# Kernel tuning notes

Hardware: AMD Instinct MI355X
Metric: run time of the kernel (lower is better)

## Reference

```python
import jax, jax.numpy as jnp
import numpy as np

D_MODEL = 1024
N_HEADS = 16
D_HEAD = 64


def setup_inputs() -> dict:
    key = jax.random.key(0)
    kx, kq, kk, kv, ko = jax.random.split(key, 5)
    B, T = 2, 2048
    inner = N_HEADS * D_HEAD
    s = 1.0 / np.sqrt(D_MODEL)
    return {
        "x": jax.random.normal(kx, (B, T, D_MODEL), dtype=jnp.float32),
        "Wq": jax.random.normal(kq, (D_MODEL, inner), dtype=jnp.float32) * s,
        "Wk": jax.random.normal(kk, (D_MODEL, inner), dtype=jnp.float32) * s,
        "Wv": jax.random.normal(kv, (D_MODEL, inner), dtype=jnp.float32) * s,
        "Wo": jax.random.normal(ko, (inner, D_MODEL), dtype=jnp.float32) * (1.0 / np.sqrt(inner)),
    }


def reference(x, Wq, Wk, Wv, Wo):
    B, T, D = x.shape
    H, d = N_HEADS, D_HEAD
    q = (x @ Wq).reshape(B, T, H, d)
    k = (x @ Wk).reshape(B, T, H, d)
    v = (x @ Wv).reshape(B, T, H, d)
    # scale=False -> no 1/sqrt(d) scaling
    scores = jnp.einsum('bthd,bshd->bhts', q, k)
    # strictly-lower-triangular mask (tril with diagonal=-1): s < t kept
    mask = jnp.tril(jnp.ones((T, T), dtype=bool), k=-1)
    scores = jnp.where(mask, scores, 0.0)
    out = jnp.einsum('bhts,bshd->bthd', scores, v).reshape(B, T, H * d)
    return out @ Wo
```

## Files before the change

### kernel.cpp

```cpp
#include <hip/hip_runtime.h>
#include <hip/hip_bf16.h>

#define TSEQ   2048
#define DM     1024
#define NHEAD  16
#define DH     64
#define BATCH  2
#define MR     (BATCH * TSEQ)
#define CH     64
#define NC     (TSEQ / CH)
#define QKVLD  (3 * DM)
#define LP     72

typedef __attribute__((ext_vector_type(8))) short bf16x8;
typedef __attribute__((ext_vector_type(4))) float f32x4;

__device__ __forceinline__ short f2bf(float x) {
  __hip_bfloat16 h = __float2bfloat16(x);
  return *reinterpret_cast<short*>(&h);
}

__device__ __forceinline__ void stage16(const void* g, void* l) {
  __builtin_amdgcn_global_load_lds(
      (const __attribute__((address_space(1))) void*)g,
      (__attribute__((address_space(3))) void*)l, 16, 0, 0);
}

__global__ __launch_bounds__(256) void gemm_qkv(const short* __restrict__ A,
                                                const short* __restrict__ Bt,
                                                short* __restrict__ qb,
                                                short* __restrict__ kb,
                                                short* __restrict__ kT,
                                                short* __restrict__ vT) {
  const int K = DM;
  __shared__ short As[128][32];
  __shared__ short Bs[128][32];
  const int tid = threadIdx.x;
  const int lane = tid & 63, wid = tid >> 6;
  const int wave_m = wid >> 1, wave_n = wid & 1;
  const int row0 = blockIdx.y * 128, col0 = blockIdx.x * 128;

  const int sr = tid >> 2, sk = (tid & 3) * 8;
  const short* Ag0 = A + (size_t)(row0 + sr) * K + sk;
  const short* Bg0 = Bt + (size_t)(col0 + sr) * K + sk;
  short* AsL = &As[0][0] + tid * 8;
  short* BsL = &Bs[0][0] + tid * 8;

  f32x4 acc[4][4];
#pragma unroll
  for (int i = 0; i < 4; ++i)
#pragma unroll
    for (int j = 0; j < 4; ++j) acc[i][j] = (f32x4){0.f, 0.f, 0.f, 0.f};

  const int fm = wave_m * 64 + (lane & 15);
  const int fn = wave_n * 64 + (lane & 15);
  const int fk = (lane >> 4) * 8;

  for (int k0 = 0; k0 < K; k0 += 32) {
    stage16(Ag0 + k0, AsL);
    stage16(Ag0 + (size_t)64 * K + k0, AsL + 2048);
    stage16(Bg0 + k0, BsL);
    stage16(Bg0 + (size_t)64 * K + k0, BsL + 2048);
    __syncthreads();
    bf16x8 af[4], bf[4];
#pragma unroll
    for (int t = 0; t < 4; ++t) {
      af[t] = *(const bf16x8*)&As[fm + t * 16][fk];
      bf[t] = *(const bf16x8*)&Bs[fn + t * 16][fk];
    }
#pragma unroll
    for (int im = 0; im < 4; ++im)
#pragma unroll
      for (int jn = 0; jn < 4; ++jn)
        acc[im][jn] = __builtin_amdgcn_mfma_f32_16x16x32_bf16(af[im], bf[jn], acc[im][jn], 0, 0, 0);
    __syncthreads();
  }

  const int crow = (lane >> 4) * 4, ccol = lane & 15;
  const int region = col0 >> 10;

  if (region <= 1) {
    short* Cb = (region == 0) ? qb : kb;
#pragma unroll
    for (int im = 0; im < 4; ++im)
#pragma unroll
      for (int jn = 0; jn < 4; ++jn) {
        const int gr = row0 + wave_m * 64 + im * 16 + crow;
        const int gc = (col0 & 1023) + wave_n * 64 + jn * 16 + ccol;
        short* Cp = Cb + (size_t)gr * DM + gc;
#pragma unroll
        for (int r = 0; r < 4; ++r) Cp[(size_t)r * DM] = f2bf(acc[im][jn][r]);
      }
  }
  if (region >= 1) {
    short* Tt = (region == 1) ? kT : vT;
    const int gr0 = row0 + wave_m * 64;
    const int b = gr0 >> 11;
    const int c = (gr0 & 2047) >> 6;
#pragma unroll
    for (int im = 0; im < 4; ++im)
#pragma unroll
      for (int jn = 0; jn < 4; ++jn) {
        const int gcol = (col0 & 1023) + wave_n * 64 + jn * 16 + ccol;
        const int h = gcol >> 6, i = gcol & 63;
        const int s0 = im * 16 + crow;
        size_t idx = ((((size_t)(b * NHEAD + h) * NC + c) * DH + i) * DH + s0);
        union { short h4[4]; uint2 u; } pk;
#pragma unroll
        for (int r = 0; r < 4; ++r) pk.h4[r] = f2bf(acc[im][jn][r]);
        *(uint2*)(Tt + idx) = pk.u;
      }
  }
}

__global__ __launch_bounds__(256) void gemm_out(const short* __restrict__ A,
                                                const short* __restrict__ Bt,
                                                float* __restrict__ C) {
  const int K = DM, N = DM;
  __shared__ short As[128][32];
  __shared__ short Bs[128][32];
  const int tid = threadIdx.x;
  const int lane = tid & 63, wid = tid >> 6;
  const int wave_m = wid >> 1, wave_n = wid & 1;
  const int row0 = blockIdx.y * 128, col0 = blockIdx.x * 128;

  const int sr = tid >> 2, sk = (tid & 3) * 8;
  const short* Ag0 = A + (size_t)(row0 + sr) * K + sk;
  const short* Bg0 = Bt + (size_t)(col0 + sr) * K + sk;
  short* AsL = &As[0][0] + tid * 8;
  short* BsL = &Bs[0][0] + tid * 8;

  f32x4 acc[4][4];
#pragma unroll
  for (int i = 0; i < 4; ++i)
#pragma unroll
    for (int j = 0; j < 4; ++j) acc[i][j] = (f32x4){0.f, 0.f, 0.f, 0.f};

  const int fm = wave_m * 64 + (lane & 15);
  const int fn = wave_n * 64 + (lane & 15);
  const int fk = (lane >> 4) * 8;

  for (int k0 = 0; k0 < K; k0 += 32) {
    stage16(Ag0 + k0, AsL);
    stage16(Ag0 + (size_t)64 * K + k0, AsL + 2048);
    stage16(Bg0 + k0, BsL);
    stage16(Bg0 + (size_t)64 * K + k0, BsL + 2048);
    __syncthreads();
    bf16x8 af[4], bf[4];
#pragma unroll
    for (int t = 0; t < 4; ++t) {
      af[t] = *(const bf16x8*)&As[fm + t * 16][fk];
      bf[t] = *(const bf16x8*)&Bs[fn + t * 16][fk];
    }
#pragma unroll
    for (int im = 0; im < 4; ++im)
#pragma unroll
      for (int jn = 0; jn < 4; ++jn)
        acc[im][jn] = __builtin_amdgcn_mfma_f32_16x16x32_bf16(af[im], bf[jn], acc[im][jn], 0, 0, 0);
    __syncthreads();
  }

  const int crow = (lane >> 4) * 4, ccol = lane & 15;
#pragma unroll
  for (int im = 0; im < 4; ++im)
#pragma unroll
    for (int jn = 0; jn < 4; ++jn) {
      float* Cp = C + (size_t)(row0 + wave_m * 64 + im * 16 + crow) * N
                    + col0 + wave_n * 64 + jn * 16 + ccol;
#pragma unroll
      for (int r = 0; r < 4; ++r) Cp[(size_t)r * N] = acc[im][jn][r];
    }
}

__global__ __launch_bounds__(256) void prep(const float* __restrict__ x,
                                            const float* __restrict__ W0,
                                            const float* __restrict__ W1,
                                            const float* __restrict__ W2,
                                            const float* __restrict__ W3,
                                            __hip_bfloat16* __restrict__ xb,
                                            __hip_bfloat16* __restrict__ Wt) {
  const int tid = threadIdx.x;
  if (blockIdx.z == 4) {
    const int bid = blockIdx.y * 16 + blockIdx.x;
    const float* src = x + (size_t)bid * 16384;
    __hip_bfloat16* dst = xb + (size_t)bid * 16384;
#pragma unroll
    for (int it = 0; it < 16; ++it) {
      int i = it * 1024 + tid * 4;
      float4 v = *(const float4*)(src + i);
      union { __hip_bfloat16 h[4]; uint2 u; } pk;
      pk.h[0] = __float2bfloat16(v.x); pk.h[1] = __float2bfloat16(v.y);
      pk.h[2] = __float2bfloat16(v.z); pk.h[3] = __float2bfloat16(v.w);
      *(uint2*)(dst + i) = pk.u;
    }
    return;
  }
  const float* W = blockIdx.z == 0 ? W0 : blockIdx.z == 1 ? W1 : blockIdx.z == 2 ? W2 : W3;
  __hip_bfloat16* out = Wt + (size_t)blockIdx.z * DM * DM;
  __shared__ float tile[64][65];
  const int kt = blockIdx.y * 64, nt = blockIdx.x * 64;
  const int lr = tid >> 6, lc = tid & 63;
#pragma unroll
  for (int i = 0; i < 16; ++i) {
    int k = i * 4 + lr;
    tile[k][lc] = W[(size_t)(kt + k) * DM + nt + lc];
  }
  __syncthreads();
  const int nl = tid >> 4, k4 = (tid & 15) * 4;
#pragma unroll
  for (int i = 0; i < 4; ++i) {
    int n = i * 16 + nl;
    union { __hip_bfloat16 h[4]; uint2 u; } pk;
#pragma unroll
    for (int xx = 0; xx < 4; ++xx) pk.h[xx] = __float2bfloat16(tile[k4 + xx][n]);
    *(uint2*)(out + (size_t)(nt + n) * DM + kt + k4) = pk.u;
  }
}

__global__ __launch_bounds__(256) void chunk_kv(const short* __restrict__ kT,
                                                const short* __restrict__ vT,
                                                float* __restrict__ Mc) {
  const int c = blockIdx.x, h = blockIdx.y, b = blockIdx.z;
  const size_t tile = ((size_t)(b * NHEAD + h) * NC + c) * (DH * DH);
  const int tid = threadIdx.x, lane = tid & 63, w = tid >> 6;
  const int m = lane & 15, q = lane >> 4;
  const short* vt = vT + tile;
  const short* kt = kT + tile;
  bf16x8 a0 = *(const bf16x8*)(vt + (16 * w + m) * DH + q * 8);
  bf16x8 a1 = *(const bf16x8*)(vt + (16 * w + m) * DH + q * 8 + 32);
  f32x4 acc[4];
#pragma unroll
  for (int ct = 0; ct < 4; ++ct) acc[ct] = (f32x4){0.f, 0.f, 0.f, 0.f};
#pragma unroll
  for (int ct = 0; ct < 4; ++ct) {
    bf16x8 b0 = *(const bf16x8*)(kt + (ct * 16 + m) * DH + q * 8);
    bf16x8 b1 = *(const bf16x8*)(kt + (ct * 16 + m) * DH + q * 8 + 32);
    acc[ct] = __builtin_amdgcn_mfma_f32_16x16x32_bf16(a0, b0, acc[ct], 0, 0, 0);
    acc[ct] = __builtin_amdgcn_mfma_f32_16x16x32_bf16(a1, b1, acc[ct], 0, 0, 0);
  }
  float* out = Mc + tile;
#pragma unroll
  for (int ct = 0; ct < 4; ++ct)
#pragma unroll
    for (int rr = 0; rr < 4; ++rr)
      out[(size_t)(16 * w + q * 4 + rr) * DH + ct * 16 + m] = acc[ct][rr];
}

__global__ __launch_bounds__(256) void scan_states(const float* __restrict__ Mc,
                                                   __hip_bfloat16* __restrict__ Spre) {
  const int bh = blockIdx.y;
  const size_t off = (size_t)bh * NC * (DH * DH) + blockIdx.x * 256 + threadIdx.x;
  const float* src = Mc + off;
  __hip_bfloat16* dst = Spre + off;
  float run = 0.f;
  for (int c = 0; c < NC; ++c) {
    dst[(size_t)c * (DH * DH)] = __float2bfloat16(run);
    run += src[(size_t)c * (DH * DH)];
  }
}

__global__ __launch_bounds__(256) void intra_attn(const short* __restrict__ qb,
                                                  const short* __restrict__ kb,
                                                  const short* __restrict__ vT,
                                                  const short* __restrict__ Spre,
                                                  short* __restrict__ O_) {
  const int c = blockIdx.x, h = blockIdx.y, b = blockIdx.z;
  __shared__ short Qs[CH][LP];
  __shared__ short Ks[CH][LP];
  const int tid = threadIdx.x, lane = tid & 63, w = tid >> 6;
  const int m = lane & 15, q = lane >> 4;
  const int r = tid >> 2, q16 = (tid & 3) * 16;
  const size_t tile = ((size_t)(b * NHEAD + h) * NC + c) * (DH * DH);
  const size_t grow = ((size_t)(b * TSEQ + c * CH + r)) * DM + h * DH;
  *(bf16x8*)&Qs[r][q16]     = *(const bf16x8*)(qb + grow + q16);
  *(bf16x8*)&Qs[r][q16 + 8] = *(const bf16x8*)(qb + grow + q16 + 8);
  *(bf16x8*)&Ks[r][q16]     = *(const bf16x8*)(kb + grow + q16);
  *(bf16x8*)&Ks[r][q16 + 8] = *(const bf16x8*)(kb + grow + q16 + 8);
  const short* vt = vT + tile;
  const short* st = Spre + tile;
  bf16x8 av0 = *(const bf16x8*)(vt + (16 * w + m) * DH + q * 8);
  bf16x8 av1 = *(const bf16x8*)(vt + (16 * w + m) * DH + q * 8 + 32);
  bf16x8 as0 = *(const bf16x8*)(st + (16 * w + m) * DH + q * 8);
  bf16x8 as1 = *(const bf16x8*)(st + (16 * w + m) * DH + q * 8 + 32);
  __syncthreads();

  bf16x8 aq0 = *(const bf16x8*)&Qs[16 * w + m][q * 8];
  bf16x8 aq1 = *(const bf16x8*)&Qs[16 * w + m][q * 8 + 32];

  f32x4 acc[4], pacc[4];
#pragma unroll
  for (int ct = 0; ct < 4; ++ct) {
    acc[ct] = (f32x4){0.f, 0.f, 0.f, 0.f};
    pacc[ct] = (f32x4){0.f, 0.f, 0.f, 0.f};
  }
#pragma unroll
  for (int ct = 0; ct < 4; ++ct) {
    bf16x8 bq0 = *(const bf16x8*)&Qs[ct * 16 + m][q * 8];
    bf16x8 bq1 = *(const bf16x8*)&Qs[ct * 16 + m][q * 8 + 32];
    acc[ct] = __builtin_amdgcn_mfma_f32_16x16x32_bf16(as0, bq0, acc[ct], 0, 0, 0);
    acc[ct] = __builtin_amdgcn_mfma_f32_16x16x32_bf16(as1, bq1, acc[ct], 0, 0, 0);
    bf16x8 bk0 = *(const bf16x8*)&Ks[ct * 16 + m][q * 8];
    bf16x8 bk1 = *(const bf16x8*)&Ks[ct * 16 + m][q * 8 + 32];
    pacc[ct] = __builtin_amdgcn_mfma_f32_16x16x32_bf16(aq0, bk0, pacc[ct], 0, 0, 0);
    pacc[ct] = __builtin_amdgcn_mfma_f32_16x16x32_bf16(aq1, bk1, pacc[ct], 0, 0, 0);
  }
  __syncthreads();
#pragma unroll
  for (int ct = 0; ct < 4; ++ct) {
    const int s = ct * 16 + m;
#pragma unroll
    for (int rr = 0; rr < 4; ++rr) {
      const int t = 16 * w + q * 4 + rr;
      Ks[t][s] = f2bf((s < t) ? pacc[ct][rr] : 0.f);
    }
  }
  __syncthreads();
#pragma unroll
  for (int ct = 0; ct < 4; ++ct) {
    bf16x8 bp0 = *(const bf16x8*)&Ks[ct * 16 + m][q * 8];
    bf16x8 bp1 = *(const bf16x8*)&Ks[ct * 16 + m][q * 8 + 32];
    acc[ct] = __builtin_amdgcn_mfma_f32_16x16x32_bf16(av0, bp0, acc[ct], 0, 0, 0);
    acc[ct] = __builtin_amdgcn_mfma_f32_16x16x32_bf16(av1, bp1, acc[ct], 0, 0, 0);
  }
#pragma unroll
  for (int ct = 0; ct < 4; ++ct) {
    const int t = ct * 16 + m, j0 = 16 * w + q * 4;
    union { short h4[4]; uint2 u; } pk;
#pragma unroll
    for (int rr = 0; rr < 4; ++rr) pk.h4[rr] = f2bf(acc[ct][rr]);
    *(uint2*)(O_ + ((size_t)(b * TSEQ + c * CH + t)) * DM + h * DH + j0) = pk.u;
  }
}

extern "C" void kernel_launch(void* const* d_in, const int* in_sizes, int n_in,
                              void* d_out, int out_size, void* d_ws, size_t ws_size,
                              hipStream_t stream) {
  const float* x  = (const float*)d_in[0];
  const float* Wq = (const float*)d_in[1];
  const float* Wk = (const float*)d_in[2];
  const float* Wv = (const float*)d_in[3];
  const float* Wo = (const float*)d_in[4];
  float* out = (float*)d_out;

  char* ws = (char*)d_ws;
  short* xb    = (short*)ws;  ws += (size_t)MR * DM * 2;
  short* WtAll = (short*)ws;  ws += (size_t)4 * DM * DM * 2;
  short* qb    = (short*)ws;  ws += (size_t)MR * DM * 2;
  short* kb    = (short*)ws;  ws += (size_t)MR * DM * 2;
  short* kT    = (short*)ws;  ws += (size_t)MR * DM * 2;
  short* vT    = (short*)ws;  ws += (size_t)MR * DM * 2;
  float* Mc    = (float*)ws;  ws += (size_t)MR * DM * 4;
  short* Spre  = (short*)ws;  ws += (size_t)MR * DM * 2;
  short* aob   = (short*)ws;  ws += (size_t)MR * DM * 2;

  prep<<<dim3(16, 16, 5), 256, 0, stream>>>(x, Wq, Wk, Wv, Wo,
                                            (__hip_bfloat16*)xb, (__hip_bfloat16*)WtAll);

  gemm_qkv<<<dim3(QKVLD / 128, MR / 128), 256, 0, stream>>>(xb, WtAll, qb, kb, kT, vT);

  chunk_kv<<<dim3(NC, NHEAD, BATCH), 256, 0, stream>>>(kT, vT, Mc);
  scan_states<<<dim3(DH * DH / 256, BATCH * NHEAD), 256, 0, stream>>>(
      Mc, (__hip_bfloat16*)Spre);
  intra_attn<<<dim3(NC, NHEAD, BATCH), 256, 0, stream>>>(qb, kb, vT, Spre, aob);

  gemm_out<<<dim3(DM / 128, MR / 128), 256, 0, stream>>>(
      aob, WtAll + (size_t)3 * DM * DM, out);
}
```

Baseline: 170.8 us.

## Fuse chunk state computation with prefix scan, deepen QKV GEMM K-step, shrink out-GEMM tile

The separate chunk_kv and scan_states kernels become one state_scan kernel. It computes each chunk's K^T V contribution with MFMA and keeps the running prefix sum in registers, so the fp32 Mc buffer no longer has to be written and read back. The QKV GEMM now stages 64 K-columns per barrier pair, halving the number of synchronisations. The output GEMM uses 128x64 tiles so twice as many blocks launch for better occupancy. The trade-off is that state_scan runs only 128 blocks that walk the chunks sequentially, which limits parallelism.

```diff
diff --git a/kernel.cpp b/kernel.cpp
--- a/kernel.cpp
+++ b/kernel.cpp
@@ -33,8 +33,8 @@
                                                 short* __restrict__ kT,
                                                 short* __restrict__ vT) {
   const int K = DM;
-  __shared__ short As[128][32];
-  __shared__ short Bs[128][32];
+  __shared__ short As[2][128][32];
+  __shared__ short Bs[2][128][32];
   const int tid = threadIdx.x;
   const int lane = tid & 63, wid = tid >> 6;
   const int wave_m = wid >> 1, wave_n = wid & 1;
@@ -43,8 +43,8 @@
   const int sr = tid >> 2, sk = (tid & 3) * 8;
   const short* Ag0 = A + (size_t)(row0 + sr) * K + sk;
   const short* Bg0 = Bt + (size_t)(col0 + sr) * K + sk;
-  short* AsL = &As[0][0] + tid * 8;
-  short* BsL = &Bs[0][0] + tid * 8;
+  short* AsL = &As[0][0][0] + tid * 8;
+  short* BsL = &Bs[0][0][0] + tid * 8;
 
   f32x4 acc[4][4];
 #pragma unroll
@@ -56,23 +56,30 @@
   const int fn = wave_n * 64 + (lane & 15);
   const int fk = (lane >> 4) * 8;
 
-  for (int k0 = 0; k0 < K; k0 += 32) {
+  for (int k0 = 0; k0 < K; k0 += 64) {
     stage16(Ag0 + k0, AsL);
     stage16(Ag0 + (size_t)64 * K + k0, AsL + 2048);
+    stage16(Ag0 + k0 + 32, AsL + 4096);
+    stage16(Ag0 + (size_t)64 * K + k0 + 32, AsL + 6144);
     stage16(Bg0 + k0, BsL);
     stage16(Bg0 + (size_t)64 * K + k0, BsL + 2048);
+    stage16(Bg0 + k0 + 32, BsL + 4096);
+    stage16(Bg0 + (size_t)64 * K + k0 + 32, BsL + 6144);
     __syncthreads();
-    bf16x8 af[4], bf[4];
-#pragma unroll
-    for (int t = 0; t < 4; ++t) {
-      af[t] = *(const bf16x8*)&As[fm + t * 16][fk];
-      bf[t] = *(const bf16x8*)&Bs[fn + t * 16][fk];
+#pragma unroll
+    for (int p = 0; p < 2; ++p) {
+      bf16x8 af[4], bf[4];
+#pragma unroll
+      for (int t = 0; t < 4; ++t) {
+        af[t] = *(const bf16x8*)&As[p][fm + t * 16][fk];
+        bf[t] = *(const bf16x8*)&Bs[p][fn + t * 16][fk];
+      }
+#pragma unroll
+      for (int im = 0; im < 4; ++im)
+#pragma unroll
+        for (int jn = 0; jn < 4; ++jn)
+          acc[im][jn] = __builtin_amdgcn_mfma_f32_16x16x32_bf16(af[im], bf[jn], acc[im][jn], 0, 0, 0);
     }
-#pragma unroll
-    for (int im = 0; im < 4; ++im)
-#pragma unroll
-      for (int jn = 0; jn < 4; ++jn)
-        acc[im][jn] = __builtin_amdgcn_mfma_f32_16x16x32_bf16(af[im], bf[jn], acc[im][jn], 0, 0, 0);
     __syncthreads();
   }
 
@@ -118,11 +125,9 @@
                                                 float* __restrict__ C) {
   const int K = DM, N = DM;
   __shared__ short As[128][32];
-  __shared__ short Bs[128][32];
-  const int tid = threadIdx.x;
-  const int lane = tid & 63, wid = tid >> 6;
-  const int wave_m = wid >> 1, wave_n = wid & 1;
-  const int row0 = blockIdx.y * 128, col0 = blockIdx.x * 128;
+  __shared__ short Bs[64][32];
+  const int tid = threadIdx.x, lane = tid & 63, wid = tid >> 6;
+  const int row0 = blockIdx.y * 128, col0 = blockIdx.x * 64;
 
   const int sr = tid >> 2, sk = (tid & 3) * 8;
   const short* Ag0 = A + (size_t)(row0 + sr) * K + sk;
@@ -130,30 +135,28 @@
   short* AsL = &As[0][0] + tid * 8;
   short* BsL = &Bs[0][0] + tid * 8;
 
-  f32x4 acc[4][4];
-#pragma unroll
-  for (int i = 0; i < 4; ++i)
+  f32x4 acc[2][4];
+#pragma unroll
+  for (int i = 0; i < 2; ++i)
 #pragma unroll
     for (int j = 0; j < 4; ++j) acc[i][j] = (f32x4){0.f, 0.f, 0.f, 0.f};
 
-  const int fm = wave_m * 64 + (lane & 15);
-  const int fn = wave_n * 64 + (lane & 15);
+  const int fm = wid * 32 + (lane & 15);
+  const int fn = lane & 15;
   const int fk = (lane >> 4) * 8;
 
   for (int k0 = 0; k0 < K; k0 += 32) {
     stage16(Ag0 + k0, AsL);
     stage16(Ag0 + (size_t)64 * K + k0, AsL + 2048);
     stage16(Bg0 + k0, BsL);
-    stage16(Bg0 + (size_t)64 * K + k0, BsL + 2048);
     __syncthreads();
-    bf16x8 af[4], bf[4];
-#pragma unroll
-    for (int t = 0; t < 4; ++t) {
-      af[t] = *(const bf16x8*)&As[fm + t * 16][fk];
-      bf[t] = *(const bf16x8*)&Bs[fn + t * 16][fk];
-    }
-#pragma unroll
-    for (int im = 0; im < 4; ++im)
+    bf16x8 af[2], bf[4];
+#pragma unroll
+    for (int t = 0; t < 2; ++t) af[t] = *(const bf16x8*)&As[fm + t * 16][fk];
+#pragma unroll
+    for (int t = 0; t < 4; ++t) bf[t] = *(const bf16x8*)&Bs[t * 16 + fn][fk];
+#pragma unroll
+    for (int im = 0; im < 2; ++im)
 #pragma unroll
       for (int jn = 0; jn < 4; ++jn)
         acc[im][jn] = __builtin_amdgcn_mfma_f32_16x16x32_bf16(af[im], bf[jn], acc[im][jn], 0, 0, 0);
@@ -162,11 +165,11 @@
 
   const int crow = (lane >> 4) * 4, ccol = lane & 15;
 #pragma unroll
-  for (int im = 0; im < 4; ++im)
+  for (int im = 0; im < 2; ++im)
 #pragma unroll
     for (int jn = 0; jn < 4; ++jn) {
-      float* Cp = C + (size_t)(row0 + wave_m * 64 + im * 16 + crow) * N
-                    + col0 + wave_n * 64 + jn * 16 + ccol;
+      float* Cp = C + (size_t)(row0 + wid * 32 + im * 16 + crow) * N
+                    + col0 + jn * 16 + ccol;
 #pragma unroll
       for (int r = 0; r < 4; ++r) Cp[(size_t)r * N] = acc[im][jn][r];
     }
@@ -217,45 +220,29 @@
   }
 }
 
-__global__ __launch_bounds__(256) void chunk_kv(const short* __restrict__ kT,
-                                                const short* __restrict__ vT,
-                                                float* __restrict__ Mc) {
-  const int c = blockIdx.x, h = blockIdx.y, b = blockIdx.z;
-  const size_t tile = ((size_t)(b * NHEAD + h) * NC + c) * (DH * DH);
+__global__ __launch_bounds__(256) void state_scan(const short* __restrict__ kT,
+                                                  const short* __restrict__ vT,
+                                                  short* __restrict__ Spre) {
+  const int js = blockIdx.x, h = blockIdx.y, b = blockIdx.z;
   const int tid = threadIdx.x, lane = tid & 63, w = tid >> 6;
   const int m = lane & 15, q = lane >> 4;
-  const short* vt = vT + tile;
-  const short* kt = kT + tile;
-  bf16x8 a0 = *(const bf16x8*)(vt + (16 * w + m) * DH + q * 8);
-  bf16x8 a1 = *(const bf16x8*)(vt + (16 * w + m) * DH + q * 8 + 32);
-  f32x4 acc[4];
-#pragma unroll
-  for (int ct = 0; ct < 4; ++ct) acc[ct] = (f32x4){0.f, 0.f, 0.f, 0.f};
-#pragma unroll
-  for (int ct = 0; ct < 4; ++ct) {
-    bf16x8 b0 = *(const bf16x8*)(kt + (ct * 16 + m) * DH + q * 8);
-    bf16x8 b1 = *(const bf16x8*)(kt + (ct * 16 + m) * DH + q * 8 + 32);
-    acc[ct] = __builtin_amdgcn_mfma_f32_16x16x32_bf16(a0, b0, acc[ct], 0, 0, 0);
-    acc[ct] = __builtin_amdgcn_mfma_f32_16x16x32_bf16(a1, b1, acc[ct], 0, 0, 0);
-  }
-  float* out = Mc + tile;
-#pragma unroll
-  for (int ct = 0; ct < 4; ++ct)
+  const size_t hbase = ((size_t)(b * NHEAD + h) * NC) * (DH * DH);
+  const int jrow = 16 * js + m;
+  const int irow = 16 * w + m;
+  f32x4 run = (f32x4){0.f, 0.f, 0.f, 0.f};
+  for (int c = 0; c < NC; ++c) {
+    const size_t tile = hbase + (size_t)c * (DH * DH);
 #pragma unroll
     for (int rr = 0; rr < 4; ++rr)
-      out[(size_t)(16 * w + q * 4 + rr) * DH + ct * 16 + m] = acc[ct][rr];
-}
-
-__global__ __launch_bounds__(256) void scan_states(const float* __restrict__ Mc,
-                                                   __hip_bfloat16* __restrict__ Spre) {
-  const int bh = blockIdx.y;
-  const size_t off = (size_t)bh * NC * (DH * DH) + blockIdx.x * 256 + threadIdx.x;
-  const float* src = Mc + off;
-  __hip_bfloat16* dst = Spre + off;
-  float run = 0.f;
-  for (int c = 0; c < NC; ++c) {
-    dst[(size_t)c * (DH * DH)] = __float2bfloat16(run);
-    run += src[(size_t)c * (DH * DH)];
+      Spre[tile + (size_t)(16 * js + q * 4 + rr) * DH + 16 * w + m] = f2bf(run[rr]);
+    bf16x8 a0 = *(const bf16x8*)(vT + tile + (size_t)jrow * DH + q * 8);
+    bf16x8 a1 = *(const bf16x8*)(vT + tile + (size_t)jrow * DH + q * 8 + 32);
+    bf16x8 b0 = *(const bf16x8*)(kT + tile + (size_t)irow * DH + q * 8);
+    bf16x8 b1 = *(const bf16x8*)(kT + tile + (size_t)irow * DH + q * 8 + 32);
+    f32x4 t = (f32x4){0.f, 0.f, 0.f, 0.f};
+    t = __builtin_amdgcn_mfma_f32_16x16x32_bf16(a0, b0, t, 0, 0, 0);
+    t = __builtin_amdgcn_mfma_f32_16x16x32_bf16(a1, b1, t, 0, 0, 0);
+    run += t;
   }
 }
 
@@ -349,7 +336,6 @@
   short* kb    = (short*)ws;  ws += (size_t)MR * DM * 2;
   short* kT    = (short*)ws;  ws += (size_t)MR * DM * 2;
   short* vT    = (short*)ws;  ws += (size_t)MR * DM * 2;
-  float* Mc    = (float*)ws;  ws += (size_t)MR * DM * 4;
   short* Spre  = (short*)ws;  ws += (size_t)MR * DM * 2;
   short* aob   = (short*)ws;  ws += (size_t)MR * DM * 2;
 
@@ -358,11 +344,10 @@
 
   gemm_qkv<<<dim3(QKVLD / 128, MR / 128), 256, 0, stream>>>(xb, WtAll, qb, kb, kT, vT);
 
-  chunk_kv<<<dim3(NC, NHEAD, BATCH), 256, 0, stream>>>(kT, vT, Mc);
-  scan_states<<<dim3(DH * DH / 256, BATCH * NHEAD), 256, 0, stream>>>(
-      Mc, (__hip_bfloat16*)Spre);
+  state_scan<<<dim3(4, NHEAD, BATCH), 256, 0, stream>>>(kT, vT, Spre);
+
   intra_attn<<<dim3(NC, NHEAD, BATCH), 256, 0, stream>>>(qb, kb, vT, Spre, aob);
 
-  gemm_out<<<dim3(DM / 128, MR / 128), 256, 0, stream>>>(
+  gemm_out<<<dim3(DM / 64, MR / 128), 256, 0, stream>>>(
       aob, WtAll + (size_t)3 * DM * DM, out);
 }
```

After: 174.3 us. +2.0%, slower.
